# Optimization experiments

Measured on AMD Instinct MI355X. Metric: run time of the kernel, lower is better.

The kernel has to match this reference:

```python
import jax, jax.numpy as jnp
import numpy as np

N_EMBD = 1024
N_HEAD = 16
HEAD_DIM = N_EMBD // N_HEAD


def setup_inputs() -> dict:
    key = jax.random.key(0)
    kx, kq, kk, kv, kp = jax.random.split(key, 5)
    B, S = 4, 2048
    x = jax.random.normal(kx, (B, S, N_EMBD), dtype=jnp.float32)
    # nn.Linear(n, n, bias=False): weight [out, in], y = x @ W.T
    s = 1.0 / np.sqrt(N_EMBD)
    Wq = jax.random.uniform(kq, (N_EMBD, N_EMBD), jnp.float32, -s, s)
    Wk = jax.random.uniform(kk, (N_EMBD, N_EMBD), jnp.float32, -s, s)
    Wv = jax.random.uniform(kv, (N_EMBD, N_EMBD), jnp.float32, -s, s)
    Wo = jax.random.uniform(kp, (N_EMBD, N_EMBD), jnp.float32, -s, s)
    return {"x": x, "Wq": Wq, "Wk": Wk, "Wv": Wv, "Wo": Wo}


def _split_heads(t):
    B, S, _ = t.shape
    return t.reshape(B, S, N_HEAD, HEAD_DIM).transpose(0, 2, 1, 3)  # [B,H,S,D]


def reference(x, Wq, Wk, Wv, Wo):
    q = _split_heads(x @ Wq.T)
    k = _split_heads(x @ Wk.T)
    v = _split_heads(x @ Wv.T)
    scale = 1.0 / np.sqrt(HEAD_DIM)
    scores = jnp.einsum('bhqd,bhkd->bhqk', q, k) * scale  # [B,H,S,S]
    S = x.shape[1]
    mask = jnp.tril(jnp.ones((S, S), dtype=bool))
    masked = jnp.where(mask[None, None], scores, -jnp.inf)
    attn = jax.nn.softmax(masked, axis=-1)
    heads = jnp.einsum('bhqk,bhkd->bhqd', attn, v)
    merged = heads.transpose(0, 2, 1, 3).reshape(x.shape[0], S, N_EMBD)
    return merged @ Wo.T
```

## Files before the change

### kernel.cpp

```cpp
#include <hip/hip_runtime.h>
#include <hip/hip_bf16.h>

typedef __hip_bfloat16 bf16;
typedef __attribute__((ext_vector_type(8))) short short8;
typedef __attribute__((ext_vector_type(4))) float f32x4;
typedef unsigned int uint32;

#define MFMA16(a, b, c) __builtin_amdgcn_mfma_f32_16x16x32_bf16(a, b, c, 0, 0, 0)

constexpr int EMB   = 1024;
constexpr int SEQ   = 2048;
constexpr int BATCH = 4;
constexpr int NH    = 16;
constexpr int HD    = 64;
constexpr int QKVW  = 3 * EMB;
constexpr float QSCALE = 0.125f * 1.44269504f;

__device__ __forceinline__ void gl_lds16(const bf16* g, bf16* l) {
    __builtin_amdgcn_global_load_lds(
        (const __attribute__((address_space(1))) void*)g,
        (__attribute__((address_space(3))) void*)l,
        16, 0, 0);
}

__device__ __forceinline__ float fexp2(float x) {
#if __has_builtin(__builtin_amdgcn_exp2f)
    return __builtin_amdgcn_exp2f(x);
#else
    return exp2f(x);
#endif
}

__device__ __forceinline__ uint32 pack2(float a, float b) {
    uint32 ua = __builtin_bit_cast(uint32, a) + 0x8000u;
    uint32 ub = __builtin_bit_cast(uint32, b) + 0x8000u;
    return __builtin_amdgcn_perm(ub, ua, 0x07060302u);
}

__device__ __forceinline__ bf16 fbf16(float f) {
    unsigned short u =
        (unsigned short)((__builtin_bit_cast(uint32, f) + 0x8000u) >> 16);
    return __builtin_bit_cast(bf16, u);
}

__device__ __forceinline__ int ps_dw(int row, int cd) {
    return row * 64 + ((((cd >> 2) ^ (row & 7)) << 3) + ((cd & 3) << 1));
}

__global__ void convert_all(const float* __restrict__ x,
                            const float* __restrict__ wq,
                            const float* __restrict__ wk,
                            const float* __restrict__ wv,
                            const float* __restrict__ wo,
                            bf16* __restrict__ xc,
                            bf16* __restrict__ wqkv,
                            bf16* __restrict__ woc) {
    const int NX = BATCH * SEQ * EMB;
    const int NW = EMB * EMB;
    const float* src; bf16* dst; int n4, b0, nb;
    const int blk = blockIdx.x;
    if (blk < 2048)      { src = x;  dst = xc;          n4 = NX / 4; b0 = 0;    nb = 2048; }
    else if (blk < 2304) { src = wq; dst = wqkv;        n4 = NW / 4; b0 = 2048; nb = 256; }
    else if (blk < 2560) { src = wk; dst = wqkv + NW;   n4 = NW / 4; b0 = 2304; nb = 256; }
    else if (blk < 2816) { src = wv; dst = wqkv + 2*NW; n4 = NW / 4; b0 = 2560; nb = 256; }
    else                 { src = wo; dst = woc;         n4 = NW / 4; b0 = 2816; nb = 256; }
    for (int i = (blk - b0) * 256 + threadIdx.x; i < n4; i += nb * 256) {
        float4 v = ((const float4*)src)[i];
        uint2 o;
        o.x = pack2(v.x, v.y);
        o.y = pack2(v.z, v.w);
        ((uint2*)dst)[i] = o;
    }
}

template <typename OutT>
__global__ __launch_bounds__(256) void gemm_bt(const bf16* __restrict__ A,
                                               const bf16* __restrict__ B,
                                               OutT* __restrict__ C,
                                               int M, int N, int K,
                                               float oscale, int qlim) {
    __shared__ __align__(16) bf16 As[128 * 64];
    __shared__ __align__(16) bf16 Bs[128 * 64];

    const int t    = threadIdx.x;
    const int lane = t & 63;
    const int wid  = t >> 6;
    const int l16  = lane & 15;
    const int quad = lane >> 4;
    const int e    = l16 & 7;
    const int wm   = (wid >> 1) * 64;
    const int wn   = (wid & 1) * 64;

    const int nwg = (int)gridDim.x;
    const int cpx = nwg >> 3;
    const int wg  = ((int)blockIdx.x & 7) * cpx + ((int)blockIdx.x >> 3);
    const int gx  = N >> 7;
    const int m0  = (wg / gx) * 128;
    const int n0  = (wg % gx) * 128;
    const float sc = (n0 < qlim) ? oscale : 1.0f;

    f32x4 acc[4][4] = {};
    const int srow = lane >> 3;
    const int scol = ((lane & 7) ^ srow) * 8;

    for (int k0 = 0; k0 < K; k0 += 64) {
        #pragma unroll
        for (int it = 0; it < 4; ++it) {
            int rb = it * 32 + wid * 8;
            gl_lds16(&A[(size_t)(m0 + rb + srow) * K + k0 + scol], &As[rb * 64]);
            gl_lds16(&B[(size_t)(n0 + rb + srow) * K + k0 + scol], &Bs[rb * 64]);
        }
        __syncthreads();
        #pragma unroll
        for (int ks = 0; ks < 64; ks += 32) {
            const int cb = (ks >> 3) + quad;
            short8 af[4], bfr[4];
            #pragma unroll
            for (int i = 0; i < 4; ++i)
                af[i] = *(const short8*)&As[(wm + i * 16 + l16) * 64 + ((cb ^ e) * 8)];
            #pragma unroll
            for (int j = 0; j < 4; ++j)
                bfr[j] = *(const short8*)&Bs[(wn + j * 16 + l16) * 64 + ((cb ^ e) * 8)];
            #pragma unroll
            for (int i = 0; i < 4; ++i)
                #pragma unroll
                for (int j = 0; j < 4; ++j)
                    acc[i][j] = MFMA16(af[i], bfr[j], acc[i][j]);
        }
        __syncthreads();
    }

    #pragma unroll
    for (int i = 0; i < 4; ++i)
        #pragma unroll
        for (int j = 0; j < 4; ++j)
            #pragma unroll
            for (int r = 0; r < 4; ++r) {
                int row = m0 + wm + i * 16 + quad * 4 + r;
                int col = n0 + wn + j * 16 + l16;
                float v = acc[i][j][r] * sc;
                if constexpr (sizeof(OutT) == 2)
                    C[(size_t)row * N + col] = fbf16(v);
                else
                    C[(size_t)row * N + col] = (OutT)v;
            }
}

__global__ __launch_bounds__(256) void transpose_v(const bf16* __restrict__ QKV,
                                                   bf16* __restrict__ Vt) {
    __shared__ __align__(16) bf16 Ts[4096];
    const int t  = threadIdx.x;
    const int st = blockIdx.x;
    const int bh = blockIdx.y;
    const int b  = bh >> 4, h = bh & 15;
    const int s0 = st * 64;

    const bf16* src = QKV + ((size_t)(b * SEQ + s0)) * QKVW + 2 * EMB + h * HD;
    {
        int r = t >> 3, cq = t & 7;
        #pragma unroll
        for (int it = 0; it < 2; ++it, r += 32) {
            uint4 v = *(const uint4*)&src[(size_t)r * QKVW + cq * 8];
            int blk = cq ^ (r >> 3);
            *(uint4*)&Ts[r * 64 + blk * 8] = v;
        }
    }
    __syncthreads();
    bf16* dst = Vt + (size_t)bh * HD * SEQ + s0;
    {
        int d = t >> 3;
        const int sq = t & 7;
        #pragma unroll
        for (int it = 0; it < 2; ++it, d += 32) {
            short8 ov;
            #pragma unroll
            for (int i = 0; i < 8; ++i) {
                int s = sq * 8 + i;
                ov[i] = (short)__bfloat16_as_ushort(
                    Ts[s * 64 + (((d >> 3) ^ sq) << 3) + (d & 7)]);
            }
            *(short8*)&dst[(size_t)d * SEQ + sq * 8] = ov;
        }
    }
}

__global__ __launch_bounds__(256) void flash_attn(const bf16* __restrict__ QKV,
                                                  const bf16* __restrict__ Vt,
                                                  bf16* __restrict__ O) {
    __shared__ __align__(16) bf16 Ks[2][64 * 64];
    __shared__ __align__(16) bf16 VTs[2][64 * 64];
    __shared__ __align__(16) bf16 Ps[4][16 * 64];

    const int t    = threadIdx.x;
    const int lane = t & 63;
    const int w    = t >> 6;
    const int l16  = lane & 15;
    const int quad = lane >> 4;
    const int e    = l16 & 7;

    const int lin = (int)blockIdx.x;
    const int wg  = ((lin & 7) << 6) + (lin >> 3);
    const int bh  = wg >> 3;
    const int pr  = wg & 7;
    const int b   = bh >> 4, h = bh & 15;

    const bf16* Qp = QKV + (size_t)b * SEQ * QKVW + h * HD;
    const bf16* Kp = QKV + (size_t)b * SEQ * QKVW + EMB + h * HD;
    const bf16* Vp = Vt + (size_t)bh * HD * SEQ;
    bf16* Op = O + (size_t)b * SEQ * EMB + h * HD;

    const int srow = lane >> 3;
    const int scol = ((lane & 7) ^ srow) * 8;

    auto stage = [&](int kt, int buf) {
        const int kbase = kt * 64;
        #pragma unroll
        for (int it = 0; it < 2; ++it) {
            int rb = it * 32 + w * 8;
            gl_lds16(&Kp[(size_t)(kbase + rb + srow) * QKVW + scol], &Ks[buf][rb * 64]);
            gl_lds16(&Vp[(size_t)(rb + srow) * SEQ + kbase + scol], &VTs[buf][rb * 64]);
        }
    };

    for (int pass = 0; pass < 2; ++pass) {
        const int qt = pass ? pr : 15 - pr;
        const int q0 = qt * 128;

        short8 bQ[2][2];
        #pragma unroll
        for (int s = 0; s < 2; ++s) {
            const size_t qr = (size_t)(q0 + w * 32 + s * 16 + l16) * QKVW;
            bQ[s][0] = *(const short8*)&Qp[qr + quad * 8];
            bQ[s][1] = *(const short8*)&Qp[qr + 32 + quad * 8];
        }

        f32x4 o[2][4] = {};
        float lrow[2] = {0.f, 0.f};

        const int ntiles = q0 / 64 + 2;

        stage(0, 0);
        stage(1, 1);

        for (int kt = 0; kt < ntiles; ++kt) {
            const int cur = kt & 1;
            const int kbase = kt * 64;
            if (kt < ntiles - 1) __builtin_amdgcn_s_waitcnt(0x0F74);
            else                 __builtin_amdgcn_s_waitcnt(0x0F70);
            __builtin_amdgcn_s_barrier();

            #pragma unroll
            for (int s = 0; s < 2; ++s) {
                const int qs0 = q0 + w * 32 + s * 16;
                if (kbase > qs0 + 15) continue;

                f32x4 sa[4];
                #pragma unroll
                for (int j = 0; j < 4; ++j) {
                    f32x4 acc = {};
                    acc = MFMA16(*(const short8*)&Ks[cur][(j * 16 + l16) * 64 + ((quad ^ e) * 8)],
                                 bQ[s][0], acc);
                    acc = MFMA16(*(const short8*)&Ks[cur][(j * 16 + l16) * 64 + (((4 + quad) ^ e) * 8)],
                                 bQ[s][1], acc);
                    sa[j] = acc;
                }

                float lsum = 0.f;
                if (kbase + 63 > qs0) {
                    #pragma unroll
                    for (int j = 0; j < 4; ++j)
                        #pragma unroll
                        for (int pp = 0; pp < 2; ++pp) {
                            int kg = kbase + j * 16 + quad * 4 + 2 * pp;
                            float e0 = fexp2(sa[j][2 * pp]);
                            float e1 = fexp2(sa[j][2 * pp + 1]);
                            float p0 = (kg     <= qs0 + l16) ? e0 : 0.f;
                            float p1 = (kg + 1 <= qs0 + l16) ? e1 : 0.f;
                            lsum += p0 + p1;
                            *(uint32*)&Ps[w][ps_dw(l16, j * 8 + quad * 2 + pp)] = pack2(p0, p1);
                        }
                } else {
                    #pragma unroll
                    for (int j = 0; j < 4; ++j)
                        #pragma unroll
                        for (int pp = 0; pp < 2; ++pp) {
                            float p0 = fexp2(sa[j][2 * pp]);
                            float p1 = fexp2(sa[j][2 * pp + 1]);
                            lsum += p0 + p1;
                            *(uint32*)&Ps[w][ps_dw(l16, j * 8 + quad * 2 + pp)] = pack2(p0, p1);
                        }
                }
                lrow[s] += lsum;

                #pragma unroll
                for (int ks = 0; ks < 2; ++ks) {
                    short8 bP = *(const short8*)&Ps[w][l16 * 64 + (((ks * 4 + quad) ^ e) << 3)];
                    #pragma unroll
                    for (int dg = 0; dg < 4; ++dg)
                        o[s][dg] = MFMA16(
                            *(const short8*)&VTs[cur][(dg * 16 + l16) * 64 + (((ks * 4 + quad) ^ e) * 8)],
                            bP, o[s][dg]);
                }
            }

            __builtin_amdgcn_s_barrier();
            if (kt + 2 < ntiles) stage(kt + 2, cur);
        }

        #pragma unroll
        for (int s = 0; s < 2; ++s) {
            float l = lrow[s];
            l += __shfl_xor(l, 16);
            l += __shfl_xor(l, 32);
            float rl = 1.0f / l;
            #pragma unroll
            for (int dg = 0; dg < 4; ++dg)
                #pragma unroll
                for (int pp = 0; pp < 2; ++pp) {
                    float v0 = o[s][dg][2 * pp] * rl;
                    float v1 = o[s][dg][2 * pp + 1] * rl;
                    *(uint32*)&Ps[w][ps_dw(l16, dg * 8 + quad * 2 + pp)] = pack2(v0, v1);
                }
            #pragma unroll
            for (int it = 0; it < 2; ++it) {
                int qr = lane >> 2;
                int ch = (lane & 3) + 4 * it;
                short8 vv = *(const short8*)&Ps[w][qr * 64 + ((ch ^ (qr & 7)) << 3)];
                *(short8*)&Op[(size_t)(q0 + w * 32 + s * 16 + qr) * EMB + ch * 8] = vv;
            }
        }
    }
}

extern "C" void kernel_launch(void* const* d_in, const int* in_sizes, int n_in,
                              void* d_out, int out_size, void* d_ws, size_t ws_size,
                              hipStream_t stream) {
    const float* x  = (const float*)d_in[0];
    const float* Wq = (const float*)d_in[1];
    const float* Wk = (const float*)d_in[2];
    const float* Wv = (const float*)d_in[3];
    const float* Wo = (const float*)d_in[4];
    float* out = (float*)d_out;
    bf16*  ws  = (bf16*)d_ws;

    const int M  = BATCH * SEQ;
    const int NX = M * EMB;
    const int NW = EMB * EMB;

    bf16* xc   = ws;
    bf16* Ab   = xc;
    bf16* Wqkv = ws + (size_t)NX;
    bf16* Woc  = Wqkv + 3 * (size_t)NW;
    bf16* QKV  = Woc + NW;
    bf16* Vt   = QKV + (size_t)M * QKVW;

    convert_all<<<3072, 256, 0, stream>>>(x, Wq, Wk, Wv, Wo, xc, Wqkv, Woc);

    gemm_bt<bf16><<<dim3((QKVW / 128) * (M / 128)), 256, 0, stream>>>(
        xc, Wqkv, QKV, M, QKVW, EMB, QSCALE, EMB);

    transpose_v<<<dim3(SEQ / 64, BATCH * NH), 256, 0, stream>>>(QKV, Vt);

    flash_attn<<<dim3((SEQ / 128) * BATCH * NH / 2), 256, 0, stream>>>(QKV, Vt, Ab);

    gemm_bt<float><<<dim3((EMB / 128) * (M / 128)), 256, 0, stream>>>(
        Ab, Woc, out, M, EMB, EMB, 1.0f, 0);
}
```

Measured before the change: 247.6 us.

## Shrink attention query tile to 64 rows and double workgroup count

The flash attention kernel now gives each wave 16 query rows instead of 32, so a workgroup covers 64 query rows per pass. The launch grid doubles to 1024 workgroups, and the block-to-work mapping and causal tile count change to match. The goal is more parallelism across CUs and finer causal load balance, with fewer registers per wave. In exchange, each K/V tile loaded into LDS is reused by half as many queries, so total K/V traffic and barrier overhead go up.

```diff
diff --git a/kernel.cpp b/kernel.cpp
--- a/kernel.cpp
+++ b/kernel.cpp
@@ -199,9 +199,9 @@
     const int e    = l16 & 7;
 
     const int lin = (int)blockIdx.x;
-    const int wg  = ((lin & 7) << 6) + (lin >> 3);
-    const int bh  = wg >> 3;
-    const int pr  = wg & 7;
+    const int wg  = ((lin & 7) << 7) + (lin >> 3);
+    const int bh  = wg >> 4;
+    const int pr  = wg & 15;
     const int b   = bh >> 4, h = bh & 15;
 
     const bf16* Qp = QKV + (size_t)b * SEQ * QKVW + h * HD;
@@ -223,24 +223,24 @@
     };
 
     for (int pass = 0; pass < 2; ++pass) {
-        const int qt = pass ? pr : 15 - pr;
-        const int q0 = qt * 128;
-
-        short8 bQ[2][2];
-        #pragma unroll
-        for (int s = 0; s < 2; ++s) {
-            const size_t qr = (size_t)(q0 + w * 32 + s * 16 + l16) * QKVW;
-            bQ[s][0] = *(const short8*)&Qp[qr + quad * 8];
-            bQ[s][1] = *(const short8*)&Qp[qr + 32 + quad * 8];
-        }
-
-        f32x4 o[2][4] = {};
-        float lrow[2] = {0.f, 0.f};
-
-        const int ntiles = q0 / 64 + 2;
+        const int qt = pass ? pr : 31 - pr;
+        const int q0 = qt * 64;
+        const int wq0 = q0 + w * 16;
+
+        short8 bQ[2];
+        {
+            const size_t qr = (size_t)(wq0 + l16) * QKVW;
+            bQ[0] = *(const short8*)&Qp[qr + quad * 8];
+            bQ[1] = *(const short8*)&Qp[qr + 32 + quad * 8];
+        }
+
+        f32x4 o[4] = {};
+        float lrow = 0.f;
+
+        const int ntiles = qt + 1;
 
         stage(0, 0);
-        stage(1, 1);
+        if (ntiles > 1) stage(1, 1);
 
         for (int kt = 0; kt < ntiles; ++kt) {
             const int cur = kt & 1;
@@ -249,67 +249,60 @@
             else                 __builtin_amdgcn_s_waitcnt(0x0F70);
             __builtin_amdgcn_s_barrier();
 
-            #pragma unroll
-            for (int s = 0; s < 2; ++s) {
-                const int qs0 = q0 + w * 32 + s * 16;
-                if (kbase > qs0 + 15) continue;
-
-                f32x4 sa[4];
-                #pragma unroll
-                for (int j = 0; j < 4; ++j) {
-                    f32x4 acc = {};
-                    acc = MFMA16(*(const short8*)&Ks[cur][(j * 16 + l16) * 64 + ((quad ^ e) * 8)],
-                                 bQ[s][0], acc);
-                    acc = MFMA16(*(const short8*)&Ks[cur][(j * 16 + l16) * 64 + (((4 + quad) ^ e) * 8)],
-                                 bQ[s][1], acc);
-                    sa[j] = acc;
-                }
-
-                float lsum = 0.f;
-                if (kbase + 63 > qs0) {
+            f32x4 sa[4];
+            #pragma unroll
+            for (int j = 0; j < 4; ++j) {
+                f32x4 acc = {};
+                acc = MFMA16(*(const short8*)&Ks[cur][(j * 16 + l16) * 64 + ((quad ^ e) * 8)],
+                             bQ[0], acc);
+                acc = MFMA16(*(const short8*)&Ks[cur][(j * 16 + l16) * 64 + (((4 + quad) ^ e) * 8)],
+                             bQ[1], acc);
+                sa[j] = acc;
+            }
+
+            float lsum = 0.f;
+            if (kbase + 63 > wq0) {
+                #pragma unroll
+                for (int j = 0; j < 4; ++j)
                     #pragma unroll
-                    for (int j = 0; j < 4; ++j)
-                        #pragma unroll
-                        for (int pp = 0; pp < 2; ++pp) {
-                            int kg = kbase + j * 16 + quad * 4 + 2 * pp;
-                            float e0 = fexp2(sa[j][2 * pp]);
-                            float e1 = fexp2(sa[j][2 * pp + 1]);
-                            float p0 = (kg     <= qs0 + l16) ? e0 : 0.f;
-                            float p1 = (kg + 1 <= qs0 + l16) ? e1 : 0.f;
-                            lsum += p0 + p1;
-                            *(uint32*)&Ps[w][ps_dw(l16, j * 8 + quad * 2 + pp)] = pack2(p0, p1);
-                        }
-                } else {
+                    for (int pp = 0; pp < 2; ++pp) {
+                        int kg = kbase + j * 16 + quad * 4 + 2 * pp;
+                        float e0 = fexp2(sa[j][2 * pp]);
+                        float e1 = fexp2(sa[j][2 * pp + 1]);
+                        float p0 = (kg     <= wq0 + l16) ? e0 : 0.f;
+                        float p1 = (kg + 1 <= wq0 + l16) ? e1 : 0.f;
+                        lsum += p0 + p1;
+                        *(uint32*)&Ps[w][ps_dw(l16, j * 8 + quad * 2 + pp)] = pack2(p0, p1);
+                    }
+            } else {
+                #pragma unroll
+                for (int j = 0; j < 4; ++j)
                     #pragma unroll
-                    for (int j = 0; j < 4; ++j)
-                        #pragma unroll
-                        for (int pp = 0; pp < 2; ++pp) {
-                            float p0 = fexp2(sa[j][2 * pp]);
-                            float p1 = fexp2(sa[j][2 * pp + 1]);
-                            lsum += p0 + p1;
-                            *(uint32*)&Ps[w][ps_dw(l16, j * 8 + quad * 2 + pp)] = pack2(p0, p1);
-                        }
-                }
-                lrow[s] += lsum;
-
-                #pragma unroll
-                for (int ks = 0; ks < 2; ++ks) {
-                    short8 bP = *(const short8*)&Ps[w][l16 * 64 + (((ks * 4 + quad) ^ e) << 3)];
-                    #pragma unroll
-                    for (int dg = 0; dg < 4; ++dg)
-                        o[s][dg] = MFMA16(
-                            *(const short8*)&VTs[cur][(dg * 16 + l16) * 64 + (((ks * 4 + quad) ^ e) * 8)],
-                            bP, o[s][dg]);
-                }
+                    for (int pp = 0; pp < 2; ++pp) {
+                        float p0 = fexp2(sa[j][2 * pp]);
+                        float p1 = fexp2(sa[j][2 * pp + 1]);
+                        lsum += p0 + p1;
+                        *(uint32*)&Ps[w][ps_dw(l16, j * 8 + quad * 2 + pp)] = pack2(p0, p1);
+                    }
+            }
+            lrow += lsum;
+
+            #pragma unroll
+            for (int ks = 0; ks < 2; ++ks) {
+                short8 bP = *(const short8*)&Ps[w][l16 * 64 + (((ks * 4 + quad) ^ e) << 3)];
+                #pragma unroll
+                for (int dg = 0; dg < 4; ++dg)
+                    o[dg] = MFMA16(
+                        *(const short8*)&VTs[cur][(dg * 16 + l16) * 64 + (((ks * 4 + quad) ^ e) * 8)],
+                        bP, o[dg]);
             }
 
             __builtin_amdgcn_s_barrier();
             if (kt + 2 < ntiles) stage(kt + 2, cur);
         }
 
-        #pragma unroll
-        for (int s = 0; s < 2; ++s) {
-            float l = lrow[s];
+        {
+            float l = lrow;
             l += __shfl_xor(l, 16);
             l += __shfl_xor(l, 32);
             float rl = 1.0f / l;
@@ -317,8 +310,8 @@
             for (int dg = 0; dg < 4; ++dg)
                 #pragma unroll
                 for (int pp = 0; pp < 2; ++pp) {
-                    float v0 = o[s][dg][2 * pp] * rl;
-                    float v1 = o[s][dg][2 * pp + 1] * rl;
+                    float v0 = o[dg][2 * pp] * rl;
+                    float v1 = o[dg][2 * pp + 1] * rl;
                     *(uint32*)&Ps[w][ps_dw(l16, dg * 8 + quad * 2 + pp)] = pack2(v0, v1);
                 }
             #pragma unroll
@@ -326,7 +319,7 @@
                 int qr = lane >> 2;
                 int ch = (lane & 3) + 4 * it;
                 short8 vv = *(const short8*)&Ps[w][qr * 64 + ((ch ^ (qr & 7)) << 3)];
-                *(short8*)&Op[(size_t)(q0 + w * 32 + s * 16 + qr) * EMB + ch * 8] = vv;
+                *(short8*)&Op[(size_t)(wq0 + qr) * EMB + ch * 8] = vv;
             }
         }
     }
@@ -361,7 +354,7 @@
 
     transpose_v<<<dim3(SEQ / 64, BATCH * NH), 256, 0, stream>>>(QKV, Vt);
 
-    flash_attn<<<dim3((SEQ / 128) * BATCH * NH / 2), 256, 0, stream>>>(QKV, Vt, Ab);
+    flash_attn<<<dim3((SEQ / 64 / 2) * BATCH * NH), 256, 0, stream>>>(QKV, Vt, Ab);
 
     gemm_bt<float><<<dim3((EMB / 128) * (M / 128)), 256, 0, stream>>>(
         Ab, Woc, out, M, EMB, EMB, 1.0f, 0);
```

Result: slower. 257.3 us (+3.9%).
